# Kernel optimization log

Hardware: AMD Instinct MI355X
Metric: run time of the kernel (lower is better)

Reference implementation:

```python
import jax, jax.numpy as jnp
import numpy as np

STRIDE = 16
MIN_SIZE = 16.0
NMS_THRESH = 0.7
N_PRE = 6000   # n_test_pre_nms
N_POST = 300   # n_test_post_nms
B, C_IN, FH, FW = 2, 256, 50, 50
A_PER = 9


def make_anchors(fh, fw):
    scales = np.array([8.0, 16.0, 32.0])
    ratios = np.array([0.5, 1.0, 2.0])
    ws, hs = [], []
    for r in ratios:
        for s in scales:
            size = s * STRIDE
            ws.append(size * np.sqrt(1.0 / r))
            hs.append(size * np.sqrt(r))
    wh = np.stack([np.array(ws), np.array(hs)], -1).reshape(1, 1, A_PER, 2)
    cx = (np.arange(fw) + 0.5) * STRIDE
    cy = (np.arange(fh) + 0.5) * STRIDE
    cyg, cxg = np.meshgrid(cy, cx, indexing='ij')
    ctr = np.stack([cxg, cyg], -1).reshape(fh, fw, 1, 2)
    anch = np.concatenate([ctr - wh / 2.0, ctr + wh / 2.0], -1)  # [fh,fw,9,4] xyxy
    return anch.reshape(-1, 4).astype(np.float32)


def conv2d(x, w, b, pad):
    y = jax.lax.conv_general_dilated(x, w, (1, 1), pad,
                                     dimension_numbers=('NCHW', 'OIHW', 'NCHW'))
    return y + b[None, :, None, None]


def decode_boxes(anchors, loc, img_w, img_h):
    # anchors [1,A,4] xyxy, loc [B,A,4] (dx,dy,dw,dh)
    aw = anchors[..., 2] - anchors[..., 0]
    ah = anchors[..., 3] - anchors[..., 1]
    acx = anchors[..., 0] + 0.5 * aw
    acy = anchors[..., 1] + 0.5 * ah
    cx = acx + loc[..., 0] * aw
    cy = acy + loc[..., 1] * ah
    w = aw * jnp.exp(loc[..., 2])
    h = ah * jnp.exp(loc[..., 3])
    x1 = jnp.clip(cx - 0.5 * w, 0.0, img_w)
    y1 = jnp.clip(cy - 0.5 * h, 0.0, img_h)
    x2 = jnp.clip(cx + 0.5 * w, 0.0, img_w)
    y2 = jnp.clip(cy + 0.5 * h, 0.0, img_h)
    return jnp.stack([x1, y1, x2, y2], -1)


def pairwise_iou(b):
    area = (b[:, 2] - b[:, 0]) * (b[:, 3] - b[:, 1])
    ix1 = jnp.maximum(b[:, None, 0], b[None, :, 0])
    iy1 = jnp.maximum(b[:, None, 1], b[None, :, 1])
    ix2 = jnp.minimum(b[:, None, 2], b[None, :, 2])
    iy2 = jnp.minimum(b[:, None, 3], b[None, :, 3])
    inter = jnp.clip(ix2 - ix1, 0.0) * jnp.clip(iy2 - iy1, 0.0)
    return inter / (area[:, None] + area[None, :] - inter)


def nms_select(boxes, scores):
    # boxes [N_PRE,4] already sorted by score descending
    iou = jax.lax.stop_gradient(pairwise_iou(boxes))
    idxs = jnp.arange(N_PRE)
    def body(i, keep):
        sup = (iou[i] > NMS_THRESH) & (idxs > i) & keep[i]
        return keep & ~sup
    keep = jax.lax.fori_loop(0, N_PRE, body, jnp.ones((N_PRE,), bool))
    keep = keep & (scores >= 0.0)          # drop invalid (score forced to -1)
    rank = jnp.cumsum(keep)
    sel = keep & (rank <= N_POST)
    order = jnp.argsort(jnp.where(sel, idxs, N_PRE))  # kept idxs first, score order
    top = order[:N_POST]
    m = jnp.arange(N_POST) < jnp.sum(sel)
    out_b = jnp.where(m[:, None], boxes[top], 0.0)
    out_s = jnp.where(m, scores[top], 0.0)
    return out_b, out_s, m


def proposal_pipeline(boxes, scores):
    # per-image: boxes [A,4], scores [A]
    valid = ((boxes[:, 2] - boxes[:, 0]) >= MIN_SIZE) & \
            ((boxes[:, 3] - boxes[:, 1]) >= MIN_SIZE)
    s = jnp.where(valid, scores, -1.0)
    top_s, top_i = jax.lax.top_k(s, N_PRE)
    return nms_select(boxes[top_i], top_s)


def setup_inputs() -> dict:
    k = jax.random.split(jax.random.key(0), 4)
    x = jax.random.normal(k[0], (B, C_IN, FH, FW), jnp.float32)
    conv1_w = 0.01 * jax.random.normal(k[1], (512, C_IN, 3, 3), jnp.float32)
    conv1_b = jnp.zeros((512,), jnp.float32)
    obj_w = 0.01 * jax.random.normal(k[2], (A_PER * 2, 512, 1, 1), jnp.float32)
    obj_b = jnp.zeros((A_PER * 2,), jnp.float32)
    loc_w = 0.01 * jax.random.normal(k[3], (A_PER * 4, 512, 1, 1), jnp.float32)
    loc_b = jnp.zeros((A_PER * 4,), jnp.float32)
    anchor_boxes = jnp.asarray(make_anchors(FH, FW))[None]  # [1, 22500, 4]
    return {"x": x, "conv1_w": conv1_w, "conv1_b": conv1_b,
            "obj_w": obj_w, "obj_b": obj_b, "loc_w": loc_w, "loc_b": loc_b,
            "anchor_boxes": anchor_boxes, "img_h": 800, "img_w": 800}


def reference(x, conv1_w, conv1_b, obj_w, obj_b, loc_w, loc_b, anchor_boxes, img_h, img_w):
    # RPN
    h = jax.nn.relu(conv2d(x, conv1_w, conv1_b, 'SAME'))
    loc = conv2d(h, loc_w, loc_b, 'VALID').transpose(0, 2, 3, 1).reshape(x.shape[0], -1, 4)
    obj = conv2d(h, obj_w, obj_b, 'VALID').transpose(0, 2, 3, 1).reshape(x.shape[0], -1, 2)
    # PreprocessHead: objectness prob, box decode, filter + sort + NMS
    scores = jax.nn.softmax(obj, axis=-1)[..., 1]                       # [B, A]
    boxes = decode_boxes(anchor_boxes[0][None], loc, float(img_w), float(img_h))  # [B, A, 4]
    out_boxes, out_scores, out_mask = jax.vmap(proposal_pipeline)(boxes, scores)
    return out_boxes, out_scores, out_mask
```

## Files before the change

kernel.cpp:

```cpp
#include <hip/hip_runtime.h>
#include <stdint.h>

#define NPOS 2500
#define NANCH 22500
#define NPRE 6000
#define NW 94
#define XPAD 2704
#define NSLOT 94
#define CMAX 32

__device__ __forceinline__ void gl_lds4(const float* g, float* l) {
  __builtin_amdgcn_global_load_lds((const __attribute__((address_space(1))) void*)g,
                                   (__attribute__((address_space(3))) void*)l, 4, 0, 0);
}
__device__ __forceinline__ void gl_lds16(const float* g, float* l) {
  __builtin_amdgcn_global_load_lds((const __attribute__((address_space(1))) void*)g,
                                   (__attribute__((address_space(3))) void*)l, 16, 0, 0);
}

__global__ __launch_bounds__(256) void prep(const float* __restrict__ w,
                                            float* __restrict__ wt,
                                            const float* __restrict__ x,
                                            float* __restrict__ xp,
                                            const float* __restrict__ objw,
                                            const float* __restrict__ locw,
                                            float* __restrict__ wt54b) {
  __shared__ float tile[32][33];
  int bid = blockIdx.x;
  int tid = threadIdx.x;
  if (bid < 1152) {
    int k0 = (bid % 72) * 32;
    int o0 = (bid / 72) * 32;
    int tx = tid & 31;
    int ty = tid >> 5;
#pragma unroll
    for (int i = 0; i < 4; ++i) {
      int oc = o0 + ty + i * 8;
      int kp = k0 + tx;
      tile[ty + i * 8][tx] = w[(size_t)oc * 2304 + kp];
    }
    __syncthreads();
#pragma unroll
    for (int i = 0; i < 4; ++i) {
      int kp = k0 + ty + i * 8;
      int ic = kp / 9, tap = kp % 9;
      wt[((size_t)tap * 256 + ic) * 512 + (o0 + tx)] = tile[tx][ty + i * 8];
    }
  } else if (bid < 6560) {
    int t = (bid - 1152) * 256 + tid;
    if (t < 2 * 256 * XPAD) {
      int c = t / XPAD;
      int r = t % XPAD;
      int yy = r / 52, xx = r % 52;
      float v = 0.f;
      if (yy >= 1 && yy <= 50 && xx >= 1 && xx <= 50)
        v = x[(size_t)c * NPOS + (yy - 1) * 50 + (xx - 1)];
      xp[t] = v;
    }
  } else {
    int t = (bid - 6560) * 256 + tid;
    if (t < 54 * 512) {
      int oc = t / 512, k = t % 512;
      float v = (oc < 18) ? objw[(size_t)oc * 512 + k] : locw[(size_t)(oc - 18) * 512 + k];
      wt54b[((size_t)(k >> 2) * 64 + oc) * 4 + (k & 3)] = v;
    }
  }
}

__global__ __launch_bounds__(256) void conv1_gemm(const float* __restrict__ xp,
                                                  const float* __restrict__ wt,
                                                  const float* __restrict__ bias,
                                                  float* __restrict__ h) {
  __shared__ __align__(16) float As[32][64];
  __shared__ __align__(16) float Bs[32][64];
  int b = blockIdx.z;
  int m0 = blockIdx.x * 64;
  int oc0 = blockIdx.y * 64;
  int tid = threadIdx.x;
  int lane = tid & 63;
  int wv = tid >> 6;
  int tn = tid & 15, tm = tid >> 4;
  float acc[4][4] = {};

  int p = m0 + lane;
  int pc = p < NPOS ? p : (NPOS - 1);
  int py = pc / 50, px = pc % 50;
  const float* gA0 = xp + (size_t)b * 256 * XPAD + py * 52 + px + 53;
  int brow = lane >> 4, bcol4 = (lane & 15) * 4;

  for (int tap = 0; tap < 9; ++tap) {
    int ky = tap / 3 - 1, kx = tap % 3 - 1;
    int koff = ky * 52 + kx;
    for (int icc = 0; icc < 8; ++icc) {
      int ic0 = icc * 32;
      __syncthreads();
#pragma unroll
      for (int j = 0; j < 8; ++j) {
        int kk = wv * 8 + j;
        gl_lds4(gA0 + (size_t)(ic0 + kk) * XPAD + koff, &As[kk][0]);
      }
#pragma unroll
      for (int q = 0; q < 2; ++q) {
        int r0 = wv * 8 + q * 4;
        gl_lds16(wt + ((size_t)tap * 256 + ic0 + r0 + brow) * 512 + oc0 + bcol4,
                 &Bs[r0][0]);
      }
      __syncthreads();
#pragma unroll
      for (int kk = 0; kk < 32; ++kk) {
        float4 av = *(const float4*)&As[kk][tm * 4];
        float4 bv = *(const float4*)&Bs[kk][tn * 4];
        float am[4] = {av.x, av.y, av.z, av.w};
        float bn[4] = {bv.x, bv.y, bv.z, bv.w};
#pragma unroll
        for (int i = 0; i < 4; ++i)
#pragma unroll
          for (int j = 0; j < 4; ++j) acc[i][j] = fmaf(am[i], bn[j], acc[i][j]);
      }
    }
  }
#pragma unroll
  for (int i = 0; i < 4; ++i) {
    int pp = m0 + tm * 4 + i;
    if (pp < NPOS) {
      float4 v;
      float* vp = (float*)&v;
#pragma unroll
      for (int j = 0; j < 4; ++j) {
        int oc = oc0 + tn * 4 + j;
        vp[j] = fmaxf(acc[i][j] + bias[oc], 0.f);
      }
      *(float4*)&h[((size_t)b * NPOS + pp) * 512 + oc0 + tn * 4] = v;
    }
  }
}

__global__ __launch_bounds__(64) void heads(const float* __restrict__ h,
                                            const float* __restrict__ wt54b,
                                            const float* __restrict__ objb,
                                            const float* __restrict__ locb,
                                            const float* __restrict__ anch,
                                            const int* __restrict__ imgh,
                                            const int* __restrict__ imgw,
                                            float* __restrict__ scores,
                                            float4* __restrict__ boxes) {
  __shared__ float hv[4 * 512];
  __shared__ float outs[4][64];
  int blk = blockIdx.x;
  int b = blk / 625;
  int p0 = (blk % 625) * 4;
  int lane = threadIdx.x;
  const float4* hp4 = (const float4*)(h + ((size_t)b * NPOS + p0) * 512);
  float4* hv4 = (float4*)hv;
#pragma unroll
  for (int q = 0; q < 8; ++q) hv4[lane + 64 * q] = hp4[lane + 64 * q];
  __syncthreads();
  if (lane < 54) {
    float bias0 = (lane < 18) ? objb[lane] : locb[lane - 18];
    float a0 = bias0, a1 = bias0, a2 = bias0, a3 = bias0;
    const float4* w4 = (const float4*)wt54b;
#pragma unroll 4
    for (int k = 0; k < 128; ++k) {
      float4 wv = w4[k * 64 + lane];
      float4 h0 = hv4[k], h1 = hv4[128 + k], h2 = hv4[256 + k], h3 = hv4[384 + k];
      a0 = fmaf(wv.x, h0.x, a0); a0 = fmaf(wv.y, h0.y, a0);
      a0 = fmaf(wv.z, h0.z, a0); a0 = fmaf(wv.w, h0.w, a0);
      a1 = fmaf(wv.x, h1.x, a1); a1 = fmaf(wv.y, h1.y, a1);
      a1 = fmaf(wv.z, h1.z, a1); a1 = fmaf(wv.w, h1.w, a1);
      a2 = fmaf(wv.x, h2.x, a2); a2 = fmaf(wv.y, h2.y, a2);
      a2 = fmaf(wv.z, h2.z, a2); a2 = fmaf(wv.w, h2.w, a2);
      a3 = fmaf(wv.x, h3.x, a3); a3 = fmaf(wv.y, h3.y, a3);
      a3 = fmaf(wv.z, h3.z, a3); a3 = fmaf(wv.w, h3.w, a3);
    }
    outs[0][lane] = a0; outs[1][lane] = a1; outs[2][lane] = a2; outs[3][lane] = a3;
  }
  __syncthreads();
  if (lane < 36) {
    int pi = lane / 9, a = lane % 9;
    int p = p0 + pi;
    float l0 = outs[pi][2 * a], l1 = outs[pi][2 * a + 1];
    float mx = fmaxf(l0, l1);
    float e0 = expf(l0 - mx);
    float e1 = expf(l1 - mx);
    float s = e1 / (e0 + e1);
    float d0 = outs[pi][18 + 4 * a + 0];
    float d1 = outs[pi][18 + 4 * a + 1];
    float d2 = outs[pi][18 + 4 * a + 2];
    float d3 = outs[pi][18 + 4 * a + 3];
    int ai = p * 9 + a;
    float4 A = ((const float4*)anch)[ai];
    float aw = A.z - A.x, ah = A.w - A.y;
    float acx = A.x + 0.5f * aw, acy = A.y + 0.5f * ah;
    float cx = acx + d0 * aw, cy = acy + d1 * ah;
    float w = aw * expf(d2), hh = ah * expf(d3);
    float W = (float)imgw[0], H = (float)imgh[0];
    float x1 = fminf(fmaxf(cx - 0.5f * w, 0.f), W);
    float y1 = fminf(fmaxf(cy - 0.5f * hh, 0.f), H);
    float x2 = fminf(fmaxf(cx + 0.5f * w, 0.f), W);
    float y2 = fminf(fmaxf(cy + 0.5f * hh, 0.f), H);
    bool valid = (x2 - x1 >= 16.f) && (y2 - y1 >= 16.f);
    scores[(size_t)b * NANCH + ai] = valid ? s : -1.f;
    boxes[(size_t)b * NANCH + ai] = make_float4(x1, y1, x2, y2);
  }
}

__device__ inline unsigned int mono_of(float f) {
  unsigned int u = __float_as_uint(f);
  return (u & 0x80000000u) ? ~u : (u | 0x80000000u);
}

__device__ __forceinline__ unsigned int suffix_strict(unsigned int v,
                                                      unsigned int* partw,
                                                      int tid, int lane, int wv) {
  unsigned int inc = v;
#pragma unroll
  for (int d = 1; d < 64; d <<= 1) {
    unsigned int u = __shfl_down(inc, d, 64);
    if (lane + d < 64) inc += u;
  }
  if (lane == 0) partw[wv] = inc;
  __syncthreads();
  if (tid < 16) {
    unsigned int tot = partw[tid];
    unsigned int inc2 = tot;
#pragma unroll
    for (int d = 1; d < 16; d <<= 1) {
      unsigned int u = __shfl_down(inc2, d, 64);
      if (tid + d < 16) inc2 += u;
    }
    partw[tid] = inc2 - tot;
  }
  __syncthreads();
  return partw[wv] + (inc - v);
}

__global__ __launch_bounds__(1024) void topk_sort(const float* __restrict__ scores,
                                                  const float4* __restrict__ boxes,
                                                  float* __restrict__ sscore,
                                                  float4* __restrict__ sbox) {
  int b = blockIdx.x;
  const float* sc = scores + (size_t)b * NANCH;
  __shared__ unsigned int hist[4096];
  __shared__ unsigned int part[1024];
  __shared__ unsigned short pidA[6016];
  __shared__ unsigned short pidB[6016];
  __shared__ unsigned short table[6144];
  __shared__ int res[8];
  int tid = threadIdx.x;
  int lane = tid & 63;
  int wv = tid >> 6;

  for (int i = tid; i < 4096; i += 1024) hist[i] = 0;
  __syncthreads();
  for (int i = tid; i < NANCH; i += 1024) atomicAdd(&hist[mono_of(sc[i]) >> 20], 1u);
  __syncthreads();
  {
    unsigned int h0 = hist[4 * tid], h1 = hist[4 * tid + 1];
    unsigned int h2 = hist[4 * tid + 2], h3 = hist[4 * tid + 3];
    unsigned int c = suffix_strict(h0 + h1 + h2 + h3, part, tid, lane, wv);
    const unsigned int need = NPRE;
    if (c < need && c + h3 >= need) { res[0] = 4 * tid + 3; res[1] = (int)c; }
    c += h3;
    if (c < need && c + h2 >= need) { res[0] = 4 * tid + 2; res[1] = (int)c; }
    c += h2;
    if (c < need && c + h1 >= need) { res[0] = 4 * tid + 1; res[1] = (int)c; }
    c += h1;
    if (c < need && c + h0 >= need) { res[0] = 4 * tid + 0; res[1] = (int)c; }
  }
  __syncthreads();
  int t1 = res[0], a1 = res[1];
  __syncthreads();

  for (int i = tid; i < 4096; i += 1024) hist[i] = 0;
  __syncthreads();
  for (int i = tid; i < NANCH; i += 1024) {
    unsigned int m = mono_of(sc[i]);
    if ((int)(m >> 20) == t1) atomicAdd(&hist[(m >> 8) & 0xFFF], 1u);
  }
  __syncthreads();
  {
    unsigned int h0 = hist[4 * tid], h1 = hist[4 * tid + 1];
    unsigned int h2 = hist[4 * tid + 2], h3 = hist[4 * tid + 3];
    unsigned int c = suffix_strict(h0 + h1 + h2 + h3, part, tid, lane, wv);
    const unsigned int need = (unsigned)(NPRE - a1);
    if (c < need && c + h3 >= need) { res[2] = 4 * tid + 3; res[3] = (int)c; }
    c += h3;
    if (c < need && c + h2 >= need) { res[2] = 4 * tid + 2; res[3] = (int)c; }
    c += h2;
    if (c < need && c + h1 >= need) { res[2] = 4 * tid + 1; res[3] = (int)c; }
    c += h1;
    if (c < need && c + h0 >= need) { res[2] = 4 * tid + 0; res[3] = (int)c; }
  }
  __syncthreads();
  int t2 = res[2], a2 = res[3];
  __syncthreads();

  for (int i = tid; i < 256; i += 1024) hist[i] = 0;
  __syncthreads();
  unsigned int top24 = ((unsigned int)t1 << 12) | (unsigned int)t2;
  for (int i = tid; i < NANCH; i += 1024) {
    unsigned int m = mono_of(sc[i]);
    if ((m >> 8) == top24) atomicAdd(&hist[m & 0xFF], 1u);
  }
  __syncthreads();
  {
    unsigned int hb = (tid < 256) ? hist[tid] : 0;
    unsigned int c = suffix_strict(hb, part, tid, lane, wv);
    if (tid < 256) {
      const unsigned int need = (unsigned)(NPRE - a1 - a2);
      if (c < need && c + hb >= need) {
        res[4] = tid;
        res[6] = (int)(need - c);
        res[7] = (hb == need - c) ? NANCH : -1;
      }
    }
  }
  __syncthreads();
  int t3 = res[4];
  unsigned int T = (top24 << 8) | (unsigned int)t3;
  int ties_needed = res[6];
  int idx_cut = res[7];
  __syncthreads();

  if (idx_cut < 0) {
    for (int i = tid; i < 704; i += 1024) hist[i] = 0;
    __syncthreads();
    for (int i = tid; i < NANCH; i += 1024)
      if (mono_of(sc[i]) == T) atomicAdd(&hist[i >> 5], 1u);
    __syncthreads();
    if (tid == 0) {
      int c = 0, cut = NANCH;
      for (int bin = 0; bin < 704; ++bin) {
        int hc = (int)hist[bin];
        if (c + hc >= ties_needed) {
          int c2 = c;
          for (int idx = bin * 32; idx < bin * 32 + 32; ++idx) {
            if (idx < NANCH && mono_of(sc[idx]) == T) {
              ++c2;
              if (c2 == ties_needed) { cut = idx; break; }
            }
          }
          break;
        }
        c += hc;
      }
      res[7] = cut;
    }
    __syncthreads();
    idx_cut = res[7];
    __syncthreads();
  }

  int base0 = tid * 22;
  unsigned int selm = 0;
  int cnt = 0;
  for (int k = 0; k < 22; ++k) {
    int i = base0 + k;
    if (i < NANCH) {
      unsigned int m = mono_of(sc[i]);
      if (m > T || (m == T && i <= idx_cut)) { selm |= 1u << k; ++cnt; }
    }
  }
  {
    int inc = cnt;
#pragma unroll
    for (int d = 1; d < 64; d <<= 1) {
      int u = __shfl_up(inc, d, 64);
      if (lane >= d) inc += u;
    }
    if (lane == 63) part[wv] = (unsigned int)inc;
    __syncthreads();
    if (tid < 16) {
      int v = (int)part[tid];
      int inc2 = v;
#pragma unroll
      for (int d = 1; d < 16; d <<= 1) {
        int u = __shfl_up(inc2, d, 16);
        if (tid >= d) inc2 += u;
      }
      part[tid] = (unsigned int)(inc2 - v);
    }
    __syncthreads();
    int pos = (int)part[wv] + (inc - cnt);
    for (int k = 0; k < 22; ++k)
      if ((selm >> k) & 1u) pidA[pos++] = (unsigned short)(base0 + k);
  }
  __syncthreads();

  unsigned short* src = pidA;
  unsigned short* dst = pidB;
  for (int pass = 0; pass < 6; ++pass) {
    int shift = pass * 6;
    for (int i = tid; i < 6144; i += 1024) table[i] = 0;
    __syncthreads();
    int dig[6], irk[6], pidr[6];
#pragma unroll
    for (int k = 0; k < 6; ++k) {
      dig[k] = 0; irk[k] = 0; pidr[k] = 0;
      int s = wv + 16 * k;
      if (s < NSLOT) {
        int e = s * 64 + lane;
        bool act = e < NPRE;
        int pid = act ? (int)src[e] : 0;
        unsigned int key = act ? ~mono_of(sc[pid]) : 0u;
        int d = (int)((key >> shift) & 63u);
        uint64_t peers = __ballot(act);
#pragma unroll
        for (int bb = 0; bb < 6; ++bb) {
          uint64_t bl = __ballot(((d >> bb) & 1) != 0);
          peers &= ((d >> bb) & 1) ? bl : ~bl;
        }
        if (act) {
          dig[k] = d;
          pidr[k] = pid;
          irk[k] = (int)__popcll(peers & ((1ull << lane) - 1ull));
          int leader = __ffsll((long long)peers) - 1;
          if (lane == leader)
            table[d * NSLOT + s] = (unsigned short)__popcll(peers);
        }
      }
    }
    __syncthreads();
    {
      int t6 = tid * 6;
      int v0 = table[t6], v1 = table[t6 + 1], v2 = table[t6 + 2];
      int v3 = table[t6 + 3], v4 = table[t6 + 4], v5 = table[t6 + 5];
      int lsum = v0 + v1 + v2 + v3 + v4 + v5;
      int inc = lsum;
#pragma unroll
      for (int d = 1; d < 64; d <<= 1) {
        int u = __shfl_up(inc, d, 64);
        if (lane >= d) inc += u;
      }
      if (lane == 63) part[wv] = (unsigned int)inc;
      __syncthreads();
      if (tid < 16) {
        int v = (int)part[tid];
        int inc2 = v;
#pragma unroll
        for (int d = 1; d < 16; d <<= 1) {
          int u = __shfl_up(inc2, d, 16);
          if (tid >= d) inc2 += u;
        }
        part[tid] = (unsigned int)(inc2 - v);
      }
      __syncthreads();
      int run = (int)part[wv] + (inc - lsum);
      table[t6] = (unsigned short)run; run += v0;
      table[t6 + 1] = (unsigned short)run; run += v1;
      table[t6 + 2] = (unsigned short)run; run += v2;
      table[t6 + 3] = (unsigned short)run; run += v3;
      table[t6 + 4] = (unsigned short)run; run += v4;
      table[t6 + 5] = (unsigned short)run;
    }
    __syncthreads();
#pragma unroll
    for (int k = 0; k < 6; ++k) {
      int s = wv + 16 * k;
      if (s < NSLOT) {
        int e = s * 64 + lane;
        if (e < NPRE) {
          int pos = (int)table[dig[k] * NSLOT + s] + irk[k];
          dst[pos] = (unsigned short)pidr[k];
        }
      }
    }
    __syncthreads();
    unsigned short* tmp = src; src = dst; dst = tmp;
  }

  for (int r = tid; r < NPRE; r += 1024) {
    int idx = (int)src[r];
    sscore[(size_t)b * NPRE + r] = sc[idx];
    sbox[(size_t)b * NPRE + r] = boxes[(size_t)b * NANCH + idx];
  }
}

__device__ __forceinline__ void iou_tile(const float4* __restrict__ sbox,
                                         uint64_t* __restrict__ M,
                                         int b, int it, int jt, int tid,
                                         float4* bi, float4* bj) {
  if (tid < 64) {
    int i = it * 64 + tid;
    bi[tid] = (i < NPRE) ? sbox[(size_t)b * NPRE + i] : make_float4(0, 0, 0, 0);
  }
  {
    int j = jt * 256 + tid;
    bj[tid] = (j < NPRE) ? sbox[(size_t)b * NPRE + j] : make_float4(0, 0, 0, 0);
  }
  __syncthreads();
  int li = tid & 63, wq = tid >> 6;
  int i = it * 64 + li;
  int w = jt * 4 + wq;
  if (i < NPRE && w < NW) {
    float4 A = bi[li];
    float areaA = (A.z - A.x) * (A.w - A.y);
    uint64_t bits = 0;
#pragma unroll 8
    for (int jj = 0; jj < 64; ++jj) {
      int j = w * 64 + jj;
      float4 Bx = bj[wq * 64 + jj];
      float ix1 = fmaxf(A.x, Bx.x), iy1 = fmaxf(A.y, Bx.y);
      float ix2 = fminf(A.z, Bx.z), iy2 = fminf(A.w, Bx.w);
      float inter = fmaxf(ix2 - ix1, 0.f) * fmaxf(iy2 - iy1, 0.f);
      float areaB = (Bx.z - Bx.x) * (Bx.w - Bx.y);
      float iou = inter / (areaA + areaB - inter);
      if ((j > i) && (j < NPRE) && (iou > 0.7f)) bits |= (1ull << jj);
    }
    M[((size_t)b * NPRE + i) * NW + w] = bits;
  }
}

__global__ __launch_bounds__(256) void iou_mat(const float4* __restrict__ sbox,
                                               uint64_t* __restrict__ M) {
  __shared__ float4 bi[64];
  __shared__ float4 bj[256];
  iou_tile(sbox, M, blockIdx.z, blockIdx.x, blockIdx.y, threadIdx.x, bi, bj);
}

__global__ __launch_bounds__(256) void iou_rest(const float4* __restrict__ sbox,
                                                uint64_t* __restrict__ M,
                                                const unsigned int* __restrict__ state) {
  if (state[blockIdx.z * 192 + 189]) return;
  int it = blockIdx.x, jt = blockIdx.y;
  if (it < CMAX && jt < CMAX / 4) return;
  __shared__ float4 bi[64];
  __shared__ float4 bj[256];
  iou_tile(sbox, M, blockIdx.z, it, jt, threadIdx.x, bi, bj);
}

__device__ inline uint64_t shfl64(uint64_t v, int src) {
  int lo = __shfl((int)(unsigned int)(v & 0xFFFFFFFFull), src, 64);
  int hi = __shfl((int)(unsigned int)(v >> 32), src, 64);
  return ((uint64_t)(unsigned int)hi << 32) | (unsigned int)lo;
}

__device__ __forceinline__ void nms_chunk(const uint64_t* __restrict__ Mb,
                                          const float* __restrict__ sscore,
                                          uint64_t* __restrict__ keep,
                                          int b, int c, int tid, int wlimit,
                                          unsigned int* supLo, unsigned int* supHi,
                                          int* klist, int* knS, int* countS) {
  int ibase = c * 64;
  if (tid < 64) {
    int lane = tid;
    if (lane == 0) *knS = 0;
    uint64_t supc = ((uint64_t)supHi[c] << 32) | supLo[c];
    uint64_t validm = (c == NW - 1) ? ((1ull << (NPRE - (NW - 1) * 64)) - 1ull) : ~0ull;
    int pos = ibase + lane;
    uint64_t myrow = (pos < NPRE) ? Mb[(size_t)pos * NW + c] : 0ull;
    bool sval = (pos < NPRE) && (sscore[(size_t)b * NPRE + pos] >= 0.f);
    uint64_t vb = __ballot(sval);
    uint64_t cur = validm & ~supc;
    uint64_t kept = 0;
    while (cur) {
      int i = __ffsll((long long)cur) - 1;
      kept |= (1ull << i);
      cur &= ~(1ull << i);
      uint64_t row = shfl64(myrow, i);
      cur &= ~row;
    }
    if (kept & (1ull << lane)) {
      int pp = atomicAdd(knS, 1);
      klist[pp] = lane;
    }
    if (lane == 0) {
      keep[b * NW + c] = kept;
      *countS += __popcll(kept & vb);
    }
  }
  __syncthreads();
  int kn = *knS;
  for (int t = tid; t < kn * 128; t += 1024) {
    int ii = t >> 7, w = t & 127;
    if (w > c && w < wlimit) {
      uint64_t row = Mb[(size_t)(ibase + klist[ii]) * NW + w];
      unsigned int lo = (unsigned int)row;
      unsigned int hi = (unsigned int)(row >> 32);
      if (lo) atomicOr(&supLo[w], lo);
      if (hi) atomicOr(&supHi[w], hi);
    }
  }
  __syncthreads();
}

__global__ __launch_bounds__(1024) void nms_scan(const uint64_t* __restrict__ M,
                                                 const float* __restrict__ sscore,
                                                 uint64_t* __restrict__ keep,
                                                 unsigned int* __restrict__ state) {
  __shared__ unsigned int supLo[NW], supHi[NW];
  __shared__ int klist[64];
  __shared__ int knS;
  __shared__ int countS;
  int b = blockIdx.x;
  int tid = threadIdx.x;
  const uint64_t* Mb = M + (size_t)b * NPRE * NW;

  for (int w = tid; w < NW; w += 1024) {
    supLo[w] = 0;
    supHi[w] = 0;
    keep[b * NW + w] = 0;
  }
  if (tid == 0) countS = 0;
  __syncthreads();

  int done = 0;
  for (int c = 0; c < CMAX; ++c) {
    nms_chunk(Mb, sscore, keep, b, c, tid, CMAX, supLo, supHi, klist, &knS, &countS);
    if (countS >= 300) { done = 1; break; }
  }
  __syncthreads();
  unsigned int* st = state + b * 192;
  for (int w = tid; w < NW; w += 1024) { st[w] = supLo[w]; st[94 + w] = supHi[w]; }
  if (tid == 0) { st[188] = (unsigned int)countS; st[189] = (unsigned int)done; }
}

__global__ __launch_bounds__(1024) void nms_finish(const uint64_t* __restrict__ M,
                                                   const float* __restrict__ sscore,
                                                   uint64_t* __restrict__ keep,
                                                   const unsigned int* __restrict__ state,
                                                   const float4* __restrict__ sbox,
                                                   float* __restrict__ out) {
  __shared__ unsigned int supLo[NW], supHi[NW];
  __shared__ int klist[64];
  __shared__ int knS;
  __shared__ int countS;
  __shared__ int cnt[128];
  __shared__ uint64_t fw[NW];
  int b = blockIdx.x;
  int tid = threadIdx.x;
  const uint64_t* Mb = M + (size_t)b * NPRE * NW;
  const unsigned int* st = state + b * 192;

  if (!st[189]) {
    for (int w = tid; w < NW; w += 1024) { supLo[w] = st[w]; supHi[w] = st[94 + w]; }
    if (tid == 0) countS = (int)st[188];
    __syncthreads();
    for (int c = 0; c < CMAX; ++c) {
      uint64_t kw = keep[b * NW + c];
      if (!kw) continue;
      int ibase = c * 64;
      const int WREST = NW - CMAX;
      for (int t = tid; t < 64 * WREST; t += 1024) {
        int j = t / WREST;
        int w = CMAX + (t % WREST);
        if ((kw >> j) & 1ull) {
          uint64_t row = Mb[(size_t)(ibase + j) * NW + w];
          unsigned int lo = (unsigned int)row;
          unsigned int hi = (unsigned int)(row >> 32);
          if (lo) atomicOr(&supLo[w], lo);
          if (hi) atomicOr(&supHi[w], hi);
        }
      }
    }
    __syncthreads();
    for (int c = CMAX; c < NW; ++c) {
      nms_chunk(Mb, sscore, keep, b, c, tid, NW, supLo, supHi, klist, &knS, &countS);
      if (countS >= 300) break;
    }
    __threadfence();
    __syncthreads();
  }

  for (int i = tid; i < 1200; i += 1024) out[b * 1200 + i] = 0.f;
  for (int i = tid; i < 300; i += 1024) {
    out[2400 + b * 300 + i] = 0.f;
    out[3000 + b * 300 + i] = 0.f;
  }
  uint64_t w = 0;
  if (tid < NW) {
    uint64_t kw = keep[b * NW + tid];
    while (kw) {
      int j = __ffsll((long long)kw) - 1;
      kw &= kw - 1;
      if (sscore[(size_t)b * NPRE + tid * 64 + j] >= 0.f) w |= (1ull << j);
    }
    fw[tid] = w;
  }
  if (tid < 128) cnt[tid] = (tid < NW) ? __popcll(w) : 0;
  __syncthreads();
  for (int off = 1; off < 128; off <<= 1) {
    int v = 0, u = 0;
    if (tid < 128) {
      v = cnt[tid];
      u = (tid >= off) ? cnt[tid - off] : 0;
    }
    __syncthreads();
    if (tid < 128) cnt[tid] = v + u;
    __syncthreads();
  }
  if (tid < NW) {
    int base = cnt[tid] - __popcll(fw[tid]);
    uint64_t ww = fw[tid];
    while (ww) {
      int j = __ffsll((long long)ww) - 1;
      ww &= ww - 1;
      if (base < 300) {
        int p = tid * 64 + j;
        float4 bx = sbox[(size_t)b * NPRE + p];
        float* ob = out + b * 1200 + base * 4;
        ob[0] = bx.x; ob[1] = bx.y; ob[2] = bx.z; ob[3] = bx.w;
        out[2400 + b * 300 + base] = sscore[(size_t)b * NPRE + p];
        out[3000 + b * 300 + base] = 1.0f;
      }
      ++base;
    }
  }
}

extern "C" void kernel_launch(void* const* d_in, const int* in_sizes, int n_in,
                              void* d_out, int out_size, void* d_ws, size_t ws_size,
                              hipStream_t stream) {
  const float* x       = (const float*)d_in[0];
  const float* conv1_w = (const float*)d_in[1];
  const float* conv1_b = (const float*)d_in[2];
  const float* obj_w   = (const float*)d_in[3];
  const float* obj_b   = (const float*)d_in[4];
  const float* loc_w   = (const float*)d_in[5];
  const float* loc_b   = (const float*)d_in[6];
  const float* anch    = (const float*)d_in[7];
  const int*   img_h   = (const int*)d_in[8];
  const int*   img_w   = (const int*)d_in[9];

  char* base = (char*)d_ws;
  float*        wt     = (float*)(base + 0);
  float*        h      = (float*)(base + 4718592);
  uint64_t*     M      = (uint64_t*)(base + 4718592);
  float*        scores = (float*)(base + 14958592);
  float4*       boxes  = (float4*)(base + 15138592);
  float*        sscore = (float*)(base + 15858592);
  float4*       sbox   = (float4*)(base + 15906592);
  uint64_t*     keep   = (uint64_t*)(base + 16098592);
  float*        xp     = (float*)(base + 16100096);
  unsigned int* state  = (unsigned int*)(base + 21637888);
  float*        wt54b  = (float*)(base + 15906592);

  hipLaunchKernelGGL(prep, dim3(6668), dim3(256), 0, stream,
                     conv1_w, wt, x, xp, obj_w, loc_w, wt54b);
  hipLaunchKernelGGL(conv1_gemm, dim3(40, 8, 2), dim3(256), 0, stream, xp, wt, conv1_b, h);
  hipLaunchKernelGGL(heads, dim3(1250), dim3(64), 0, stream, h, wt54b, obj_b, loc_b,
                     anch, img_h, img_w, scores, boxes);
  hipLaunchKernelGGL(topk_sort, dim3(2), dim3(1024), 0, stream, scores, boxes, sscore, sbox);
  hipLaunchKernelGGL(iou_mat, dim3(CMAX, CMAX / 4, 2), dim3(256), 0, stream, sbox, M);
  hipLaunchKernelGGL(nms_scan, dim3(2), dim3(1024), 0, stream, M, sscore, keep, state);
  hipLaunchKernelGGL(iou_rest, dim3(NW, 24, 2), dim3(256), 0, stream, sbox, M, state);
  hipLaunchKernelGGL(nms_finish, dim3(2), dim3(1024), 0, stream, M, sscore, keep, state,
                     sbox, (float*)d_out);
}
```

Baseline: 425.2 us.

## Sort only top 2048 candidates first, run full top-6000 sort only when NMS needs it

The top-k sort is templated on selection size. A fast version selects and sorts only the top 2048 scores before the first IoU/NMS scan. A gated full 6000-element sort runs after the scan and exits early when the scan state says 300 proposals were already found. This removes most radix-sort work in the common case, at the cost of an extra launch and a dependency on the state flag layout written by nms_scan.

```diff
diff --git a/kernel.cpp b/kernel.cpp
--- a/kernel.cpp
+++ b/kernel.cpp
@@ -6,8 +6,8 @@
 #define NPRE 6000
 #define NW 94
 #define XPAD 2704
-#define NSLOT 94
 #define CMAX 32
+#define KFAST 2048
 
 __device__ __forceinline__ void gl_lds4(const float* g, float* l) {
   __builtin_amdgcn_global_load_lds((const __attribute__((address_space(1))) void*)g,
@@ -234,17 +234,20 @@
   return partw[wv] + (inc - v);
 }
 
-__global__ __launch_bounds__(1024) void topk_sort(const float* __restrict__ scores,
-                                                  const float4* __restrict__ boxes,
-                                                  float* __restrict__ sscore,
-                                                  float4* __restrict__ sbox) {
+template <int KSEL, int SLOTK, int TBLSZ, bool GATED>
+__global__ __launch_bounds__(1024) void topk_sort_t(const float* __restrict__ scores,
+                                                    const float4* __restrict__ boxes,
+                                                    float* __restrict__ sscore,
+                                                    float4* __restrict__ sbox,
+                                                    const unsigned int* __restrict__ state) {
   int b = blockIdx.x;
+  if (GATED && state[b * 192 + 189]) return;
   const float* sc = scores + (size_t)b * NANCH;
   __shared__ unsigned int hist[4096];
   __shared__ unsigned int part[1024];
-  __shared__ unsigned short pidA[6016];
-  __shared__ unsigned short pidB[6016];
-  __shared__ unsigned short table[6144];
+  __shared__ unsigned short pidA[SLOTK * 64];
+  __shared__ unsigned short pidB[SLOTK * 64];
+  __shared__ unsigned short table[TBLSZ];
   __shared__ int res[8];
   int tid = threadIdx.x;
   int lane = tid & 63;
@@ -258,7 +261,7 @@
     unsigned int h0 = hist[4 * tid], h1 = hist[4 * tid + 1];
     unsigned int h2 = hist[4 * tid + 2], h3 = hist[4 * tid + 3];
     unsigned int c = suffix_strict(h0 + h1 + h2 + h3, part, tid, lane, wv);
-    const unsigned int need = NPRE;
+    const unsigned int need = KSEL;
     if (c < need && c + h3 >= need) { res[0] = 4 * tid + 3; res[1] = (int)c; }
     c += h3;
     if (c < need && c + h2 >= need) { res[0] = 4 * tid + 2; res[1] = (int)c; }
@@ -282,7 +285,7 @@
     unsigned int h0 = hist[4 * tid], h1 = hist[4 * tid + 1];
     unsigned int h2 = hist[4 * tid + 2], h3 = hist[4 * tid + 3];
     unsigned int c = suffix_strict(h0 + h1 + h2 + h3, part, tid, lane, wv);
-    const unsigned int need = (unsigned)(NPRE - a1);
+    const unsigned int need = (unsigned)(KSEL - a1);
     if (c < need && c + h3 >= need) { res[2] = 4 * tid + 3; res[3] = (int)c; }
     c += h3;
     if (c < need && c + h2 >= need) { res[2] = 4 * tid + 2; res[3] = (int)c; }
@@ -307,7 +310,7 @@
     unsigned int hb = (tid < 256) ? hist[tid] : 0;
     unsigned int c = suffix_strict(hb, part, tid, lane, wv);
     if (tid < 256) {
-      const unsigned int need = (unsigned)(NPRE - a1 - a2);
+      const unsigned int need = (unsigned)(KSEL - a1 - a2);
       if (c < need && c + hb >= need) {
         res[4] = tid;
         res[6] = (int)(need - c);
@@ -389,18 +392,20 @@
 
   unsigned short* src = pidA;
   unsigned short* dst = pidB;
+  constexpr int KITER = (SLOTK + 15) / 16;
+  constexpr int VPT = TBLSZ / 1024;
   for (int pass = 0; pass < 6; ++pass) {
     int shift = pass * 6;
-    for (int i = tid; i < 6144; i += 1024) table[i] = 0;
-    __syncthreads();
-    int dig[6], irk[6], pidr[6];
-#pragma unroll
-    for (int k = 0; k < 6; ++k) {
+    for (int i = tid; i < TBLSZ; i += 1024) table[i] = 0;
+    __syncthreads();
+    int dig[KITER], irk[KITER], pidr[KITER];
+#pragma unroll
+    for (int k = 0; k < KITER; ++k) {
       dig[k] = 0; irk[k] = 0; pidr[k] = 0;
       int s = wv + 16 * k;
-      if (s < NSLOT) {
+      if (s < SLOTK) {
         int e = s * 64 + lane;
-        bool act = e < NPRE;
+        bool act = e < KSEL;
         int pid = act ? (int)src[e] : 0;
         unsigned int key = act ? ~mono_of(sc[pid]) : 0u;
         int d = (int)((key >> shift) & 63u);
@@ -416,16 +421,17 @@
           irk[k] = (int)__popcll(peers & ((1ull << lane) - 1ull));
           int leader = __ffsll((long long)peers) - 1;
           if (lane == leader)
-            table[d * NSLOT + s] = (unsigned short)__popcll(peers);
+            table[d * SLOTK + s] = (unsigned short)__popcll(peers);
         }
       }
     }
     __syncthreads();
     {
-      int t6 = tid * 6;
-      int v0 = table[t6], v1 = table[t6 + 1], v2 = table[t6 + 2];
-      int v3 = table[t6 + 3], v4 = table[t6 + 4], v5 = table[t6 + 5];
-      int lsum = v0 + v1 + v2 + v3 + v4 + v5;
+      int tb = tid * VPT;
+      int v[VPT];
+      int lsum = 0;
+#pragma unroll
+      for (int q = 0; q < VPT; ++q) { v[q] = table[tb + q]; lsum += v[q]; }
       int inc = lsum;
 #pragma unroll
       for (int d = 1; d < 64; d <<= 1) {
@@ -435,32 +441,28 @@
       if (lane == 63) part[wv] = (unsigned int)inc;
       __syncthreads();
       if (tid < 16) {
-        int v = (int)part[tid];
-        int inc2 = v;
+        int vv = (int)part[tid];
+        int inc2 = vv;
 #pragma unroll
         for (int d = 1; d < 16; d <<= 1) {
           int u = __shfl_up(inc2, d, 16);
           if (tid >= d) inc2 += u;
         }
-        part[tid] = (unsigned int)(inc2 - v);
+        part[tid] = (unsigned int)(inc2 - vv);
       }
       __syncthreads();
       int run = (int)part[wv] + (inc - lsum);
-      table[t6] = (unsigned short)run; run += v0;
-      table[t6 + 1] = (unsigned short)run; run += v1;
-      table[t6 + 2] = (unsigned short)run; run += v2;
-      table[t6 + 3] = (unsigned short)run; run += v3;
-      table[t6 + 4] = (unsigned short)run; run += v4;
-      table[t6 + 5] = (unsigned short)run;
-    }
-    __syncthreads();
-#pragma unroll
-    for (int k = 0; k < 6; ++k) {
+#pragma unroll
+      for (int q = 0; q < VPT; ++q) { table[tb + q] = (unsigned short)run; run += v[q]; }
+    }
+    __syncthreads();
+#pragma unroll
+    for (int k = 0; k < KITER; ++k) {
       int s = wv + 16 * k;
-      if (s < NSLOT) {
+      if (s < SLOTK) {
         int e = s * 64 + lane;
-        if (e < NPRE) {
-          int pos = (int)table[dig[k] * NSLOT + s] + irk[k];
+        if (e < KSEL) {
+          int pos = (int)table[dig[k] * SLOTK + s] + irk[k];
           dst[pos] = (unsigned short)pidr[k];
         }
       }
@@ -469,7 +471,7 @@
     unsigned short* tmp = src; src = dst; dst = tmp;
   }
 
-  for (int r = tid; r < NPRE; r += 1024) {
+  for (int r = tid; r < KSEL; r += 1024) {
     int idx = (int)src[r];
     sscore[(size_t)b * NPRE + r] = sc[idx];
     sbox[(size_t)b * NPRE + r] = boxes[(size_t)b * NANCH + idx];
@@ -740,9 +742,12 @@
   hipLaunchKernelGGL(conv1_gemm, dim3(40, 8, 2), dim3(256), 0, stream, xp, wt, conv1_b, h);
   hipLaunchKernelGGL(heads, dim3(1250), dim3(64), 0, stream, h, wt54b, obj_b, loc_b,
                      anch, img_h, img_w, scores, boxes);
-  hipLaunchKernelGGL(topk_sort, dim3(2), dim3(1024), 0, stream, scores, boxes, sscore, sbox);
+  hipLaunchKernelGGL((topk_sort_t<KFAST, 32, 2048, false>), dim3(2), dim3(1024), 0, stream,
+                     scores, boxes, sscore, sbox, state);
   hipLaunchKernelGGL(iou_mat, dim3(CMAX, CMAX / 4, 2), dim3(256), 0, stream, sbox, M);
   hipLaunchKernelGGL(nms_scan, dim3(2), dim3(1024), 0, stream, M, sscore, keep, state);
+  hipLaunchKernelGGL((topk_sort_t<NPRE, 94, 6144, true>), dim3(2), dim3(1024), 0, stream,
+                     scores, boxes, sscore, sbox, state);
   hipLaunchKernelGGL(iou_rest, dim3(NW, 24, 2), dim3(256), 0, stream, sbox, M, state);
   hipLaunchKernelGGL(nms_finish, dim3(2), dim3(1024), 0, stream, M, sscore, keep, state,
                      sbox, (float*)d_out);
```

New measurement: 406.6 us, median of 2. -4.4%, faster.
